# Optimization experiments

Measured on AMD Instinct MI355X. Metric: run time of the kernel, lower is better.

## Reference

```python
import jax, jax.numpy as jnp
from jax import lax
import numpy as np

# constants from module construction: segmentation_loss3D(alpha=1.0, percentile=95)
ALPHA_T = 1.0          # tversky alpha
BETA_T = 2.0 - ALPHA_T # tversky beta
EPS = 1e-5
HD_ALPHA = 2.0         # HausdorffDTLoss default alpha
BIG = 1e9              # stand-in for +inf in the min-plus distance transform


def _dt1d(f, axis):
    """Exact 1D squared Euclidean distance transform along `axis`:
    d[i] = min_j f[j] + (i - j)^2, computed as a min-plus scan over j."""
    n = f.shape[axis]
    fT = jnp.moveaxis(f, axis, 0)                      # (n, ...)
    idx = jnp.arange(n, dtype=f.dtype)
    d0 = jnp.full(fT.shape[1:] + (n,), BIG, f.dtype)   # (..., n)

    def step(d, xs):
        fj, j = xs
        return jnp.minimum(d, fj[..., None] + (idx - j) ** 2), None

    d, _ = lax.scan(step, d0, (fT, idx))
    return jnp.moveaxis(d, -1, axis)


def _edt(mask):
    """Euclidean distance to the nearest False voxel (matches scipy edt),
    over all axes except the two leading (stack, batch) axes."""
    f = jnp.where(mask, jnp.float32(BIG), jnp.float32(0.0))
    for ax in range(2, mask.ndim):
        f = _dt1d(f, ax)
    return jnp.sqrt(f)


def _distance_fields(pred, target_oh):
    # scipy loop runs edt over the full (C, X, Y, Z) array per batch element
    imgs = jnp.stack([pred, target_oh])           # (2, B, C, X, Y, Z)
    fg = imgs > 0.5
    masks = jnp.concatenate([fg, ~fg], axis=0)    # (4, B, C, X, Y, Z)
    dist = _edt(masks)
    field = dist[:2] + dist[2:]                   # fg_dist + bg_dist
    has_fg = jnp.any(fg, axis=(2, 3, 4, 5))       # (2, B) -- torch.no_grad guard
    field = jnp.where(has_fg[:, :, None, None, None, None], field, 0.0)
    field = lax.stop_gradient(field)
    return field[0], field[1]


def setup_inputs() -> dict:
    key = jax.random.key(0)
    k1, k2 = jax.random.split(key)
    B, C, X, Y, Z = 2, 8, 64, 64, 64
    inputs = jax.random.normal(k1, (B, C, X, Y, Z), dtype=jnp.float32)
    targets = jax.random.randint(k2, (B, X, Y, Z), 0, C, dtype=jnp.int32)
    return {"inputs": inputs, "targets": targets}


def reference(inputs, targets):
    C = inputs.shape[1]
    t_oh = jax.nn.one_hot(targets, C, axis=1, dtype=inputs.dtype)  # (B,C,X,Y,Z)

    # --- tversky (dice) loss ---
    probs = jax.nn.softmax(inputs, axis=1)
    red = tuple(range(2, inputs.ndim))
    tps = jnp.sum(probs * t_oh, red)
    fps = jnp.sum(probs * (1.0 - t_oh), red) * ALPHA_T
    fns = jnp.sum((1.0 - probs) * t_oh, red) * BETA_T
    score = 2.0 * tps / (2.0 * tps + fps + fns + EPS)   # (B, C)
    dice = 1.0 - jnp.mean(score, axis=0)[1:].mean()

    # --- cross entropy (mean over all voxels) ---
    logp = jax.nn.log_softmax(inputs, axis=1)
    ce = -jnp.mean(jnp.take_along_axis(logp, targets[:, None].astype(jnp.int32), axis=1))

    # --- Hausdorff distance-transform loss ---
    pred_dt, target_dt = _distance_fields(inputs, t_oh)
    pred_error = (inputs - t_oh) ** 2
    distance = pred_dt ** HD_ALPHA + target_dt ** HD_ALPHA
    hd = jnp.mean(pred_error * distance)

    return dice + ce + hd
```

## Files before the change

### kernel.cpp

```cpp
#include <hip/hip_runtime.h>

#define NVOX (64 * 64 * 64)
#define FMU (16 * NVOX)
#define FM (16 * NVOX)


__device__ __forceinline__ float unpack_val(unsigned short p) {
    int v = p & 0x7fff;
    return (v == 32767) ? 1e9f : (float)v;
}


__global__ __launch_bounds__(256) void k_zy2(const float* __restrict__ in,
                                             const int* __restrict__ tg,
                                             unsigned short* __restrict__ f) {
    __shared__ float tile[64 * 65];
    unsigned short* tile16 = (unsigned short*)tile;
    int blk = blockIdx.x;
    int src = blk >> 10;
    int s = blk & 1023;
    int b = s >> 9, c = (s >> 6) & 7, x = s & 63;
    int w = threadIdx.x >> 6;
    int lane = threadIdx.x & 63;

    const float* pin = in + (b * 8 + c) * NVOX + x * 4096;
    const int* ptg = tg + b * NVOX + x * 4096;

#pragma unroll
    for (int k = 0; k < 16; ++k) {
        int y = k * 4 + w;
        bool member;
        if (src == 0) member = pin[y * 64 + lane] > 0.5f;
        else          member = ptg[y * 64 + lane] == c;
        unsigned long long mkA = __ballot(!member);
        unsigned long long sm = member ? mkA : ~mkA;
        unsigned long long sf = sm << (63 - lane), sb = sm >> lane;
        int df = sf ? __builtin_clzll(sf) : 64;
        int db = sb ? __builtin_ctzll(sb) : 64;
        int dz = df < db ? df : db;
        float pv = (dz > 63) ? 1e9f : (float)(dz * dz);
        tile[y * 65 + lane] = member ? -pv : pv;
    }
    __syncthreads();

    float rA[16];
    bool mreg[16];
#pragma unroll
    for (int k = 0; k < 16; ++k) {
        int z = k * 4 + w;
        float sv = tile[lane * 65 + z];
        bool m = sv < 0.f;
        float pv = fabsf(sv);
        float msign = m ? -1.f : 1.f;
        unsigned long long mw = __ballot(m);
        unsigned long long xm = m ? ~mw : mw;
        unsigned long long sf = xm << (63 - lane), sb = xm >> lane;
        int df = sf ? __builtin_clzll(sf) : 64;
        int db = sb ? __builtin_ctzll(sb) : 64;
        int dopp = df < db ? df : db;
        float d = fminf(pv, (dopp > 63) ? 1e9f : (float)(dopp * dopp));
        int q = 1;
        for (int dd = 1; dd <= 63 && (float)q < d; ++dd) {
            int jl = lane - dd, jr = lane + dd;
            float cl = 1e9f, cr = 1e9f;
            if (jl >= 0) {
                float t = tile[jl * 65 + z] * msign;
                cl = (t > 0.f) ? t : 1e9f;
            }
            if (jr < 64) {
                float t = tile[jr * 65 + z] * msign;
                cr = (t > 0.f) ? t : 1e9f;
            }
            d = fminf(d, fminf(cl, cr) + (float)q);
            q += 2 * dd + 1;
        }
        rA[k] = fminf(d, 1e9f);
        mreg[k] = m;
    }
    __syncthreads();

#pragma unroll
    for (int k = 0; k < 16; ++k) {
        int z = k * 4 + w;
        int vi = (int)fminf(rA[k], 32767.f);
        tile16[lane * 65 + z] = (unsigned short)((mreg[k] ? 0x8000 : 0) | vi);
    }
    __syncthreads();

    unsigned short* out = f + (size_t)src * FMU + (b * 8 + c) * NVOX + x * 4096;
#pragma unroll
    for (int k = 0; k < 16; ++k) {
        int y = k * 4 + w;
        out[y * 64 + lane] = tile16[y * 65 + lane];
    }
}

__global__ __launch_bounds__(256) void k_xdt(unsigned short* __restrict__ f) {
    __shared__ float tile[64 * 65];
    unsigned short* tile16 = (unsigned short*)tile;
    int blk = blockIdx.x;
    int src = blk >> 10;
    int s = blk & 1023;
    int b = s >> 9, c = (s >> 6) & 7, y = s & 63;
    int w = threadIdx.x >> 6;
    int lane = threadIdx.x & 63;

    unsigned short* base = f + (size_t)src * FMU + (b * 8 + c) * NVOX + y * 64;

#pragma unroll
    for (int k = 0; k < 16; ++k) {
        int x = k * 4 + w;
        unsigned short p = base[x * 4096 + lane];
        float v = unpack_val(p);
        tile[x * 65 + lane] = (p & 0x8000) ? -v : v;
    }
    __syncthreads();

    float rA[16];
    bool mreg[16];
#pragma unroll
    for (int k = 0; k < 16; ++k) {
        int z = k * 4 + w;
        float sv = tile[lane * 65 + z];
        bool m = sv < 0.f;
        float pv = fabsf(sv);
        float msign = m ? -1.f : 1.f;
        unsigned long long mw = __ballot(m);
        unsigned long long xm = m ? ~mw : mw;
        unsigned long long sf = xm << (63 - lane), sb = xm >> lane;
        int df = sf ? __builtin_clzll(sf) : 64;
        int db = sb ? __builtin_ctzll(sb) : 64;
        int dopp = df < db ? df : db;
        float d = fminf(pv, (dopp > 63) ? 1e9f : (float)(dopp * dopp));
        int q = 1;
        for (int dd = 1; dd <= 63 && (float)q < d; ++dd) {
            int jl = lane - dd, jr = lane + dd;
            float cl = 1e9f, cr = 1e9f;
            if (jl >= 0) {
                float t = tile[jl * 65 + z] * msign;
                cl = (t > 0.f) ? t : 1e9f;
            }
            if (jr < 64) {
                float t = tile[jr * 65 + z] * msign;
                cr = (t > 0.f) ? t : 1e9f;
            }
            d = fminf(d, fminf(cl, cr) + (float)q);
            q += 2 * dd + 1;
        }
        rA[k] = fminf(d, 1e9f);
        mreg[k] = m;
    }
    __syncthreads();

#pragma unroll
    for (int k = 0; k < 16; ++k) {
        int z = k * 4 + w;
        int vi = (int)fminf(rA[k], 32767.f);
        tile16[lane * 65 + z] = (unsigned short)((mreg[k] ? 0x8000 : 0) | vi);
    }
    __syncthreads();

#pragma unroll
    for (int k = 0; k < 16; ++k) {
        int x = k * 4 + w;
        base[x * 4096 + lane] = tile16[x * 65 + lane];
    }
}

__global__ __launch_bounds__(256) void k_chds(const float* __restrict__ in,
                                              const int* __restrict__ tg,
                                              const unsigned short* __restrict__ f,
                                              float* __restrict__ statP,
                                              double* __restrict__ predS,
                                              double* __restrict__ tgtS) {
    __shared__ float part[4][27];
    __shared__ int af;
    if (threadIdx.x == 0) af = 0;
    __syncthreads();

    int blk = blockIdx.x;
    int v = blk * 256 + threadIdx.x;
    int b = v >> 18;
    int r = v & (NVOX - 1);
    int t = tg[v];
    int lane = threadIdx.x & 63;
    int wid = threadIdx.x >> 6;

    float xs[8], ex[8];
#pragma unroll
    for (int c = 0; c < 8; ++c) xs[c] = in[(b * 8 + c) * NVOX + r];
    float mx = xs[0];
#pragma unroll
    for (int c = 1; c < 8; ++c) mx = fmaxf(mx, xs[c]);
    float se = 0.f;
#pragma unroll
    for (int c = 0; c < 8; ++c) { ex[c] = expf(xs[c] - mx); se += ex[c]; }
    float inv = 1.f / se;
    float lse = mx + logf(se);
    float xt = xs[0];
#pragma unroll
    for (int c = 1; c < 8; ++c) xt = (t == c) ? xs[c] : xt;

    bool anyP = false;
    float red[17];
    float cnt[8];
#pragma unroll
    for (int c = 0; c < 8; ++c) {
        float p = ex[c] * inv;
        red[c] = p;
        red[8 + c] = (t == c) ? p : 0.f;
        cnt[c] = (float)__popcll(__ballot(t == c));
        anyP = anyP || (xs[c] > 0.5f);
    }
    red[16] = lse - xt;

#pragma unroll
    for (int k = 0; k < 17; ++k) {
        float s = red[k];
        s += __shfl_down(s, 32);
        s += __shfl_down(s, 16);
        s += __shfl_down(s, 8);
        s += __shfl_down(s, 4);
        s += __shfl_down(s, 2);
        s += __shfl_down(s, 1);
        red[k] = s;
    }
    bool wav = __any(anyP);
    if (lane == 0) {
#pragma unroll
        for (int k = 0; k < 8; ++k) part[wid][k] = red[k];
#pragma unroll
        for (int k = 0; k < 8; ++k) part[wid][8 + k] = red[8 + k];
#pragma unroll
        for (int k = 0; k < 8; ++k) part[wid][16 + k] = cnt[k];
        part[wid][24] = red[16];
        if (wav) atomicOr(&af, 1);
    }

    float e2[8];
#pragma unroll
    for (int c = 0; c < 8; ++c) {
        float e = xs[c] - ((t == c) ? 1.f : 0.f);
        e2[c] = e * e;
    }
    float accP = 0.f, accT = 0.f;
#pragma unroll
    for (int src = 0; src < 2; ++src) {
        float fmA[8], fmB[8];
#pragma unroll
        for (int c = 0; c < 8; ++c) {
            unsigned short p = f[(size_t)src * FMU + (b * 8 + c) * NVOX + r];
            float fv = unpack_val(p);
            bool member = (p & 0x8000) != 0;
            fmA[c] = member ? fv : 0.f;
            fmB[c] = member ? 0.f : fv;
        }
        float am = 0.f;
#pragma unroll
        for (int i = 0; i < 8; ++i) {
            float da = 1e9f, db = 1e9f;
#pragma unroll
            for (int j = 0; j < 8; ++j) {
                float q = (float)((i - j) * (i - j));
                da = fminf(da, fmA[j] + q);
                db = fminf(db, fmB[j] + q);
            }
            am += e2[i] * (da + db);
        }
        if (src) accT += am; else accP += am;
    }
#pragma unroll
    for (int off = 32; off >= 1; off >>= 1) {
        accP += __shfl_down(accP, off);
        accT += __shfl_down(accT, off);
    }
    if (lane == 0) { part[wid][25] = accP; part[wid][26] = accT; }
    __syncthreads();

    int j = blk & 1023;
    if (threadIdx.x < 25)
        statP[(b * 26 + threadIdx.x) * 1024 + j] =
            part[0][threadIdx.x] + part[1][threadIdx.x] +
            part[2][threadIdx.x] + part[3][threadIdx.x];
    if (threadIdx.x == 25)
        statP[(b * 26 + 25) * 1024 + j] = af ? 1.f : 0.f;
    if (threadIdx.x == 26)
        predS[blk] = (double)part[0][25] + (double)part[1][25] +
                     (double)part[2][25] + (double)part[3][25];
    if (threadIdx.x == 27)
        tgtS[blk] = (double)part[0][26] + (double)part[1][26] +
                    (double)part[2][26] + (double)part[3][26];
}

__global__ __launch_bounds__(256) void k_final3(const float* __restrict__ statP,
                                                const double* __restrict__ predS,
                                                const double* __restrict__ tgtS,
                                                float* __restrict__ out) {
    __shared__ float rs[52];
    __shared__ double rd[4];
    int tid = threadIdx.x;
    int w = tid >> 6;
    int lane = tid & 63;

    for (int row = w; row < 52; row += 4) {
        const float* p = statP + row * 1024;
        float s = 0.f;
#pragma unroll
        for (int k = 0; k < 16; ++k) s += p[k * 64 + lane];
        s += __shfl_down(s, 32);
        s += __shfl_down(s, 16);
        s += __shfl_down(s, 8);
        s += __shfl_down(s, 4);
        s += __shfl_down(s, 2);
        s += __shfl_down(s, 1);
        if (lane == 0) rs[row] = s;
    }
    {
        const double* p = (w < 2) ? (predS + w * 1024) : (tgtS + (w - 2) * 1024);
        double s = 0.0;
#pragma unroll
        for (int k = 0; k < 16; ++k) s += p[k * 64 + lane];
        s += __shfl_down(s, 32);
        s += __shfl_down(s, 16);
        s += __shfl_down(s, 8);
        s += __shfl_down(s, 4);
        s += __shfl_down(s, 2);
        s += __shfl_down(s, 1);
        if (lane == 0) rd[w] = s;
    }
    __syncthreads();

    if (tid == 0) {
        bool fP0 = rs[0 * 26 + 25] > 0.f;
        bool fP1 = rs[1 * 26 + 25] > 0.f;
        double h = (fP0 ? rd[0] : 0.0) + (fP1 ? rd[1] : 0.0) + rd[2] + rd[3];
        float dsum = 0.f;
        for (int c = 1; c < 8; ++c) {
            float sc = 0.f;
            for (int b = 0; b < 2; ++b) {
                float S1 = rs[b * 26 + c];
                float S2 = rs[b * 26 + 8 + c];
                float Nc = rs[b * 26 + 16 + c];
                sc += 2.f * S2 / (2.f * S2 + (S1 - S2) + (Nc - S2) + 1e-5f);
            }
            dsum += sc * 0.5f;
        }
        float dice = 1.f - dsum / 7.f;
        float ce = (rs[0 * 26 + 24] + rs[1 * 26 + 24]) / 524288.f;
        out[0] = dice + ce + (float)(h / 4194304.0);
    }
}

__global__ __launch_bounds__(256, 4) void k_stats(const float* __restrict__ in,
                                                  const int* __restrict__ tg,
                                                  float* __restrict__ accF,
                                                  int* __restrict__ flags) {
    int r = blockIdx.x * 256 + threadIdx.x;
    int lane = threadIdx.x & 63;
    int wid = threadIdx.x >> 6;
    __shared__ float part[4][25];
    __shared__ int af;

    for (int b = 0; b < 2; ++b) {
        int t = tg[b * NVOX + r];
        float xs[8];
#pragma unroll
        for (int c = 0; c < 8; ++c) xs[c] = in[(b * 8 + c) * NVOX + r];
        float mx = xs[0];
#pragma unroll
        for (int c = 1; c < 8; ++c) mx = fmaxf(mx, xs[c]);
        float ex[8];
        float se = 0.f;
#pragma unroll
        for (int c = 0; c < 8; ++c) { ex[c] = expf(xs[c] - mx); se += ex[c]; }
        float inv = 1.f / se;
        float lse = mx + logf(se);
        float xt = xs[0];
#pragma unroll
        for (int c = 1; c < 8; ++c) xt = (t == c) ? xs[c] : xt;
        bool anyP = false;
        float red[25];
#pragma unroll
        for (int c = 0; c < 8; ++c) {
            float p = ex[c] * inv;
            red[c] = p;
            red[8 + c] = (t == c) ? p : 0.f;
            red[16 + c] = (t == c) ? 1.f : 0.f;
            anyP = anyP || (xs[c] > 0.5f);
        }
        red[24] = lse - xt;
#pragma unroll
        for (int k = 0; k < 25; ++k) {
            float s = red[k];
            s += __shfl_down(s, 32);
            s += __shfl_down(s, 16);
            s += __shfl_down(s, 8);
            s += __shfl_down(s, 4);
            s += __shfl_down(s, 2);
            s += __shfl_down(s, 1);
            red[k] = s;
        }
        if (threadIdx.x == 0) af = 0;
        __syncthreads();
        bool wav = __any(anyP);
        if (lane == 0) {
#pragma unroll
            for (int k = 0; k < 25; ++k) part[wid][k] = red[k];
            if (wav) atomicOr(&af, 1);
        }
        __syncthreads();
        if (threadIdx.x < 25) {
            float s = part[0][threadIdx.x] + part[1][threadIdx.x] +
                      part[2][threadIdx.x] + part[3][threadIdx.x];
            atomicAdd(&accF[b * 25 + threadIdx.x], s);
        }
        if (threadIdx.x == 0 && af) atomicOr(&flags[b], 1);
        __syncthreads();
    }
}

template <int M0>
__global__ __launch_bounds__(64) void k_mask_zy(const float* __restrict__ in,
                                                const int* __restrict__ tg,
                                                float* __restrict__ f) {
    __shared__ float tile[64 * 65];
    int blk = blockIdx.x;
    int m = M0 + (blk >> 10);
    int s = blk & 1023;
    int b = s >> 9, c = (s >> 6) & 7, x = s & 63;
    int tid = threadIdx.x;

    if ((m & 1) == 0) {
        const float* src = in + (b * 8 + c) * NVOX + x * 4096;
#pragma unroll 8
        for (int k = 0; k < 64; ++k) {
            bool fg = src[k * 64 + tid] > 0.5f;
            bool hot = (m < 2) ? fg : !fg;
            tile[k * 65 + tid] = hot ? 1e9f : 0.f;
        }
    } else {
        const int* src = tg + b * NVOX + x * 4096;
#pragma unroll 8
        for (int k = 0; k < 64; ++k) {
            bool fg = (src[k * 64 + tid] == c);
            bool hot = (m < 2) ? fg : !fg;
            tile[k * 65 + tid] = hot ? 1e9f : 0.f;
        }
    }
    __syncthreads();
    {
        float* row = &tile[tid * 65];
        float g = 1000.f;
#pragma unroll 8
        for (int z = 0; z < 64; ++z) {
            float v = row[z];
            g = (v == 0.f) ? 0.f : g + 1.f;
            row[z] = g;
        }
        g = 1000.f;
#pragma unroll 8
        for (int z = 63; z >= 0; --z) {
            float gf = row[z];
            g = (gf == 0.f) ? 0.f : g + 1.f;
            float d = fminf(gf, g);
            row[z] = (d > 63.f) ? 1e9f : d * d;
        }
    }
    __syncthreads();
    float* out = f + (size_t)(blk >> 10) * FM + (b * 8 + c) * NVOX + x * 4096;
    for (int i = 0; i < 64; ++i) {
        float d0 = tile[i * 65 + tid];
        float d = d0;
        int Ri = (int)sqrtf(d0) + 1;
        Ri = (Ri > 63) ? 63 : Ri;
        for (int dd = 1; dd <= Ri; ++dd) {
            float q = (float)(dd * dd);
            int jl = i - dd, jr = i + dd;
            float cl = (jl >= 0) ? tile[jl * 65 + tid] : 1e9f;
            float cr = (jr < 64) ? tile[jr * 65 + tid] : 1e9f;
            d = fminf(d, fminf(cl, cr) + q);
        }
        out[i * 64 + tid] = fminf(d, 1e9f);
    }
}

template <int M0>
__global__ __launch_bounds__(128, 4) void k_dtx(float* __restrict__ f) {
    __shared__ float wl[128 * 65];
    int blk = blockIdx.x;
    int mi = blk >> 9;
    int s = blk & 511;
    int plane = s >> 5;
    int y0 = (s & 31) * 2;
    int tid = threadIdx.x;
    float* fb = f + (size_t)mi * FM + plane * NVOX + y0 * 64;

#pragma unroll 8
    for (int j = 0; j < 64; ++j) wl[tid * 65 + j] = fb[j * 4096 + tid];

    float* row = &wl[tid * 65];
    for (int i = 0; i < 64; ++i) {
        float d0 = row[i];
        float d = d0;
        int Ri = (int)sqrtf(d0) + 1;
        Ri = (Ri > 63) ? 63 : Ri;
        for (int dd = 1; dd <= Ri; ++dd) {
            float q = (float)(dd * dd);
            int jl = i - dd, jr = i + dd;
            float cl = (jl >= 0) ? row[jl] : 1e9f;
            float cr = (jr < 64) ? row[jr] : 1e9f;
            d = fminf(d, fminf(cl, cr) + q);
        }
        fb[i * 4096 + tid] = fminf(d, 1e9f);
    }
}

template <int M0, int NM>
__global__ __launch_bounds__(256, 4) void k_cdt_hd(const float* __restrict__ in,
                                                   const int* __restrict__ tg,
                                                   const float* __restrict__ f,
                                                   const int* __restrict__ flags,
                                                   double* __restrict__ hd) {
    int v = blockIdx.x * 256 + threadIdx.x;
    int b = v >> 18;
    int r = v & (NVOX - 1);
    int t = tg[v];

    float e2[8];
#pragma unroll
    for (int c = 0; c < 8; ++c) {
        float e = in[(b * 8 + c) * NVOX + r] - ((t == c) ? 1.f : 0.f);
        e2[c] = e * e;
    }
    float acc = 0.f;
#pragma unroll
    for (int mi = 0; mi < NM; ++mi) {
        int m = M0 + mi;
        float fl = (m & 1) ? 1.f : (flags[b] ? 1.f : 0.f);
        float fm[8];
#pragma unroll
        for (int c = 0; c < 8; ++c)
            fm[c] = f[(size_t)mi * FM + (b * 8 + c) * NVOX + r];
        float am = 0.f;
#pragma unroll
        for (int i = 0; i < 8; ++i) {
            float d = 1e9f;
#pragma unroll
            for (int j = 0; j < 8; ++j)
                d = fminf(d, fm[j] + (float)((i - j) * (i - j)));
            am += e2[i] * d;
        }
        acc += fl * am;
    }
    float ssum = acc;
    ssum += __shfl_down(ssum, 32);
    ssum += __shfl_down(ssum, 16);
    ssum += __shfl_down(ssum, 8);
    ssum += __shfl_down(ssum, 4);
    ssum += __shfl_down(ssum, 2);
    ssum += __shfl_down(ssum, 1);
    __shared__ float part[4];
    int lane = threadIdx.x & 63;
    int wid = threadIdx.x >> 6;
    if (lane == 0) part[wid] = ssum;
    __syncthreads();
    if (threadIdx.x == 0)
        atomicAdd(hd, (double)(part[0] + part[1] + part[2] + part[3]));
}

__global__ void k_final(const float* __restrict__ accF,
                        const double* __restrict__ hd,
                        float* __restrict__ out) {
    float dsum = 0.f;
    for (int c = 1; c < 8; ++c) {
        float sc = 0.f;
        for (int b = 0; b < 2; ++b) {
            float S1 = accF[b * 25 + c];
            float S2 = accF[b * 25 + 8 + c];
            float Nc = accF[b * 25 + 16 + c];
            sc += 2.f * S2 / (2.f * S2 + (S1 - S2) + (Nc - S2) + 1e-5f);
        }
        dsum += sc * 0.5f;
    }
    float dice = 1.f - dsum / 7.f;
    float ce = (accF[24] + accF[25 + 24]) / 524288.f;
    float hdv = (float)(hd[0] / 4194304.0);
    out[0] = dice + ce + hdv;
}

template <int M0, int NM>
static void run_chunk(const float* in, const int* tg, float* f,
                      const int* flags, double* hd, hipStream_t stream) {
    k_mask_zy<M0><<<NM * 1024, 64, 0, stream>>>(in, tg, f);
    k_dtx<M0><<<NM * 512, 128, 0, stream>>>(f);
    k_cdt_hd<M0, NM><<<2048, 256, 0, stream>>>(in, tg, f, flags, hd);
}

extern "C" void kernel_launch(void* const* d_in, const int* in_sizes, int n_in,
                              void* d_out, int out_size, void* d_ws, size_t ws_size,
                              hipStream_t stream) {
    const float* in = (const float*)d_in[0];
    const int* tg = (const int*)d_in[1];
    float* out = (float*)d_out;

    size_t offF = (size_t)2 * FMU * 2;
    size_t need_fast = offF + 16384 + 16384 + 52 * 1024 * 4;

    if (ws_size >= need_fast) {
        unsigned short* fu = (unsigned short*)d_ws;
        double* predS = (double*)((char*)d_ws + offF);
        double* tgtS = (double*)((char*)d_ws + offF + 16384);
        float* statP = (float*)((char*)d_ws + offF + 32768);
        k_zy2<<<2048, 256, 0, stream>>>(in, tg, fu);
        k_xdt<<<2048, 256, 0, stream>>>(fu);
        k_chds<<<2048, 256, 0, stream>>>(in, tg, fu, statP, predS, tgtS);
        k_final3<<<1, 256, 0, stream>>>(statP, predS, tgtS, out);
    } else {
        float* f = (float*)d_ws;
        size_t acc_off = ((ws_size - 256) / 256) * 256;
        char* accB = (char*)d_ws + acc_off;
        double* hd = (double*)accB;
        float* accF = (float*)(accB + 8);
        int* flags = (int*)(accB + 208);
        hipMemsetAsync(accB, 0, 256, stream);
        k_stats<<<1024, 256, 0, stream>>>(in, tg, accF, flags);
        int nm_cap = (int)(acc_off / ((size_t)FM * 4));
        if (nm_cap >= 2) {
            run_chunk<0, 2>(in, tg, f, flags, hd, stream);
            run_chunk<2, 2>(in, tg, f, flags, hd, stream);
        } else if (nm_cap >= 1) {
            run_chunk<0, 1>(in, tg, f, flags, hd, stream);
            run_chunk<1, 1>(in, tg, f, flags, hd, stream);
            run_chunk<2, 1>(in, tg, f, flags, hd, stream);
            run_chunk<3, 1>(in, tg, f, flags, hd, stream);
        }
        k_final<<<1, 1, 0, stream>>>(accF, hd, out);
    }
}
```

Before: 141.3 us.

## Vectorize packed-field IO, drop ballot pre-pass, process two voxels per thread

The 1D distance scans in k_zy2 and k_xdt drop the ballot/clz opposite-membership pre-pass. Opposite-label neighbours now count as distance zero inside the scan loop, so the same minimum is found by iterating. Loads and stores of the 16-bit packed field now move 32-bit pairs, with the shared tile padded to 66 shorts per row to match. k_chds handles two adjacent voxels per thread using float2/int2 loads, which halves the grid and the partial-sum arrays that k_final3 reduces. The trade-off is that the scan loop may now run longer for voxels whose nearest opposite voxel is far away, and each thread in k_chds holds more registers.

Result: faster. 125.7 us (-11.1%).

```diff
diff --git a/kernel.cpp b/kernel.cpp
--- a/kernel.cpp
+++ b/kernel.cpp
@@ -52,24 +52,18 @@
         bool m = sv < 0.f;
         float pv = fabsf(sv);
         float msign = m ? -1.f : 1.f;
-        unsigned long long mw = __ballot(m);
-        unsigned long long xm = m ? ~mw : mw;
-        unsigned long long sf = xm << (63 - lane), sb = xm >> lane;
-        int df = sf ? __builtin_clzll(sf) : 64;
-        int db = sb ? __builtin_ctzll(sb) : 64;
-        int dopp = df < db ? df : db;
-        float d = fminf(pv, (dopp > 63) ? 1e9f : (float)(dopp * dopp));
+        float d = pv;
         int q = 1;
         for (int dd = 1; dd <= 63 && (float)q < d; ++dd) {
             int jl = lane - dd, jr = lane + dd;
             float cl = 1e9f, cr = 1e9f;
             if (jl >= 0) {
                 float t = tile[jl * 65 + z] * msign;
-                cl = (t > 0.f) ? t : 1e9f;
+                cl = (t > 0.f) ? t : 0.f;
             }
             if (jr < 64) {
                 float t = tile[jr * 65 + z] * msign;
-                cr = (t > 0.f) ? t : 1e9f;
+                cr = (t > 0.f) ? t : 0.f;
             }
             d = fminf(d, fminf(cl, cr) + (float)q);
             q += 2 * dd + 1;
@@ -83,15 +77,18 @@
     for (int k = 0; k < 16; ++k) {
         int z = k * 4 + w;
         int vi = (int)fminf(rA[k], 32767.f);
-        tile16[lane * 65 + z] = (unsigned short)((mreg[k] ? 0x8000 : 0) | vi);
-    }
-    __syncthreads();
-
-    unsigned short* out = f + (size_t)src * FMU + (b * 8 + c) * NVOX + x * 4096;
-#pragma unroll
-    for (int k = 0; k < 16; ++k) {
-        int y = k * 4 + w;
-        out[y * 64 + lane] = tile16[y * 65 + lane];
+        tile16[lane * 66 + z] = (unsigned short)((mreg[k] ? 0x8000 : 0) | vi);
+    }
+    __syncthreads();
+
+    unsigned int* out32 =
+        (unsigned int*)(f + (size_t)src * FMU + (b * 8 + c) * NVOX + x * 4096);
+    const unsigned int* t32 = (const unsigned int*)tile16;
+    int col = lane & 31;
+#pragma unroll
+    for (int k = 0; k < 8; ++k) {
+        int y = k * 8 + w * 2 + (lane >> 5);
+        out32[y * 32 + col] = t32[y * 33 + col];
     }
 }
 
@@ -106,13 +103,19 @@
     int lane = threadIdx.x & 63;
 
     unsigned short* base = f + (size_t)src * FMU + (b * 8 + c) * NVOX + y * 64;
-
-#pragma unroll
-    for (int k = 0; k < 16; ++k) {
-        int x = k * 4 + w;
-        unsigned short p = base[x * 4096 + lane];
-        float v = unpack_val(p);
-        tile[x * 65 + lane] = (p & 0x8000) ? -v : v;
+    unsigned int* base32 = (unsigned int*)base;
+    int col = lane & 31;
+
+#pragma unroll
+    for (int k = 0; k < 8; ++k) {
+        int x = k * 8 + w * 2 + (lane >> 5);
+        unsigned int pk = base32[x * 2048 + col];
+        unsigned short p0 = (unsigned short)(pk & 0xffff);
+        unsigned short p1 = (unsigned short)(pk >> 16);
+        float v0 = unpack_val(p0), v1 = unpack_val(p1);
+        int zz = col * 2;
+        tile[x * 65 + zz] = (p0 & 0x8000) ? -v0 : v0;
+        tile[x * 65 + zz + 1] = (p1 & 0x8000) ? -v1 : v1;
     }
     __syncthreads();
 
@@ -125,24 +128,18 @@
         bool m = sv < 0.f;
         float pv = fabsf(sv);
         float msign = m ? -1.f : 1.f;
-        unsigned long long mw = __ballot(m);
-        unsigned long long xm = m ? ~mw : mw;
-        unsigned long long sf = xm << (63 - lane), sb = xm >> lane;
-        int df = sf ? __builtin_clzll(sf) : 64;
-        int db = sb ? __builtin_ctzll(sb) : 64;
-        int dopp = df < db ? df : db;
-        float d = fminf(pv, (dopp > 63) ? 1e9f : (float)(dopp * dopp));
+        float d = pv;
         int q = 1;
         for (int dd = 1; dd <= 63 && (float)q < d; ++dd) {
             int jl = lane - dd, jr = lane + dd;
             float cl = 1e9f, cr = 1e9f;
             if (jl >= 0) {
                 float t = tile[jl * 65 + z] * msign;
-                cl = (t > 0.f) ? t : 1e9f;
+                cl = (t > 0.f) ? t : 0.f;
             }
             if (jr < 64) {
                 float t = tile[jr * 65 + z] * msign;
-                cr = (t > 0.f) ? t : 1e9f;
+                cr = (t > 0.f) ? t : 0.f;
             }
             d = fminf(d, fminf(cl, cr) + (float)q);
             q += 2 * dd + 1;
@@ -156,14 +153,15 @@
     for (int k = 0; k < 16; ++k) {
         int z = k * 4 + w;
         int vi = (int)fminf(rA[k], 32767.f);
-        tile16[lane * 65 + z] = (unsigned short)((mreg[k] ? 0x8000 : 0) | vi);
-    }
-    __syncthreads();
-
-#pragma unroll
-    for (int k = 0; k < 16; ++k) {
-        int x = k * 4 + w;
-        base[x * 4096 + lane] = tile16[x * 65 + lane];
+        tile16[lane * 66 + z] = (unsigned short)((mreg[k] ? 0x8000 : 0) | vi);
+    }
+    __syncthreads();
+
+    const unsigned int* t32 = (const unsigned int*)tile16;
+#pragma unroll
+    for (int k = 0; k < 8; ++k) {
+        int x = k * 8 + w * 2 + (lane >> 5);
+        base32[x * 2048 + col] = t32[x * 33 + col];
     }
 }
 
@@ -179,40 +177,56 @@
     __syncthreads();
 
     int blk = blockIdx.x;
-    int v = blk * 256 + threadIdx.x;
+    int v = blk * 512 + threadIdx.x * 2;
     int b = v >> 18;
     int r = v & (NVOX - 1);
-    int t = tg[v];
     int lane = threadIdx.x & 63;
     int wid = threadIdx.x >> 6;
 
-    float xs[8], ex[8];
-#pragma unroll
-    for (int c = 0; c < 8; ++c) xs[c] = in[(b * 8 + c) * NVOX + r];
-    float mx = xs[0];
-#pragma unroll
-    for (int c = 1; c < 8; ++c) mx = fmaxf(mx, xs[c]);
-    float se = 0.f;
-#pragma unroll
-    for (int c = 0; c < 8; ++c) { ex[c] = expf(xs[c] - mx); se += ex[c]; }
-    float inv = 1.f / se;
-    float lse = mx + logf(se);
-    float xt = xs[0];
-#pragma unroll
-    for (int c = 1; c < 8; ++c) xt = (t == c) ? xs[c] : xt;
-
+    int2 tt = *(const int2*)&tg[v];
+    float2 xv[8];
+#pragma unroll
+    for (int c = 0; c < 8; ++c)
+        xv[c] = *(const float2*)&in[(b * 8 + c) * NVOX + r];
+
+    float red[17];
+#pragma unroll
+    for (int k = 0; k < 17; ++k) red[k] = 0.f;
     bool anyP = false;
-    float red[17];
+
+#pragma unroll
+    for (int u = 0; u < 2; ++u) {
+        int t = u ? tt.y : tt.x;
+        float xs[8];
+#pragma unroll
+        for (int c = 0; c < 8; ++c) xs[c] = u ? xv[c].y : xv[c].x;
+        float mx = xs[0];
+#pragma unroll
+        for (int c = 1; c < 8; ++c) mx = fmaxf(mx, xs[c]);
+        float ex[8];
+        float se = 0.f;
+#pragma unroll
+        for (int c = 0; c < 8; ++c) { ex[c] = expf(xs[c] - mx); se += ex[c]; }
+        float inv = 1.f / se;
+        float lse = mx + logf(se);
+        float xt = xs[0];
+#pragma unroll
+        for (int c = 1; c < 8; ++c) xt = (t == c) ? xs[c] : xt;
+#pragma unroll
+        for (int c = 0; c < 8; ++c) {
+            float p = ex[c] * inv;
+            red[c] += p;
+            red[8 + c] += (t == c) ? p : 0.f;
+            anyP = anyP || (xs[c] > 0.5f);
+        }
+        red[16] += lse - xt;
+    }
+
     float cnt[8];
 #pragma unroll
-    for (int c = 0; c < 8; ++c) {
-        float p = ex[c] * inv;
-        red[c] = p;
-        red[8 + c] = (t == c) ? p : 0.f;
-        cnt[c] = (float)__popcll(__ballot(t == c));
-        anyP = anyP || (xs[c] > 0.5f);
-    }
-    red[16] = lse - xt;
+    for (int c = 0; c < 8; ++c)
+        cnt[c] = (float)(__popcll(__ballot(tt.x == c)) +
+                         __popcll(__ballot(tt.y == c)));
 
 #pragma unroll
     for (int k = 0; k < 17; ++k) {
@@ -237,37 +251,51 @@
         if (wav) atomicOr(&af, 1);
     }
 
-    float e2[8];
-#pragma unroll
-    for (int c = 0; c < 8; ++c) {
-        float e = xs[c] - ((t == c) ? 1.f : 0.f);
-        e2[c] = e * e;
-    }
+    unsigned int fw[16];
+#pragma unroll
+    for (int src = 0; src < 2; ++src)
+#pragma unroll
+        for (int c = 0; c < 8; ++c)
+            fw[src * 8 + c] =
+                *(const unsigned int*)&f[(size_t)src * FMU + (b * 8 + c) * NVOX + r];
+
     float accP = 0.f, accT = 0.f;
 #pragma unroll
-    for (int src = 0; src < 2; ++src) {
-        float fmA[8], fmB[8];
+    for (int u = 0; u < 2; ++u) {
+        int t = u ? tt.y : tt.x;
+        float e2[8];
 #pragma unroll
         for (int c = 0; c < 8; ++c) {
-            unsigned short p = f[(size_t)src * FMU + (b * 8 + c) * NVOX + r];
-            float fv = unpack_val(p);
-            bool member = (p & 0x8000) != 0;
-            fmA[c] = member ? fv : 0.f;
-            fmB[c] = member ? 0.f : fv;
-        }
-        float am = 0.f;
-#pragma unroll
-        for (int i = 0; i < 8; ++i) {
-            float da = 1e9f, db = 1e9f;
-#pragma unroll
-            for (int j = 0; j < 8; ++j) {
-                float q = (float)((i - j) * (i - j));
-                da = fminf(da, fmA[j] + q);
-                db = fminf(db, fmB[j] + q);
+            float x = u ? xv[c].y : xv[c].x;
+            float e = x - ((t == c) ? 1.f : 0.f);
+            e2[c] = e * e;
+        }
+#pragma unroll
+        for (int src = 0; src < 2; ++src) {
+            float fmA[8], fmB[8];
+#pragma unroll
+            for (int c = 0; c < 8; ++c) {
+                unsigned int pk = fw[src * 8 + c];
+                unsigned short p = (unsigned short)(u ? (pk >> 16) : (pk & 0xffff));
+                float fv = unpack_val(p);
+                bool member = (p & 0x8000) != 0;
+                fmA[c] = member ? fv : 0.f;
+                fmB[c] = member ? 0.f : fv;
             }
-            am += e2[i] * (da + db);
-        }
-        if (src) accT += am; else accP += am;
+            float am = 0.f;
+#pragma unroll
+            for (int i = 0; i < 8; ++i) {
+                float da = 1e9f, db = 1e9f;
+#pragma unroll
+                for (int j = 0; j < 8; ++j) {
+                    float q = (float)((i - j) * (i - j));
+                    da = fminf(da, fmA[j] + q);
+                    db = fminf(db, fmB[j] + q);
+                }
+                am += e2[i] * (da + db);
+            }
+            if (src) accT += am; else accP += am;
+        }
     }
 #pragma unroll
     for (int off = 32; off >= 1; off >>= 1) {
@@ -277,13 +305,13 @@
     if (lane == 0) { part[wid][25] = accP; part[wid][26] = accT; }
     __syncthreads();
 
-    int j = blk & 1023;
+    int j = blk & 511;
     if (threadIdx.x < 25)
-        statP[(b * 26 + threadIdx.x) * 1024 + j] =
+        statP[(b * 26 + threadIdx.x) * 512 + j] =
             part[0][threadIdx.x] + part[1][threadIdx.x] +
             part[2][threadIdx.x] + part[3][threadIdx.x];
     if (threadIdx.x == 25)
-        statP[(b * 26 + 25) * 1024 + j] = af ? 1.f : 0.f;
+        statP[(b * 26 + 25) * 512 + j] = af ? 1.f : 0.f;
     if (threadIdx.x == 26)
         predS[blk] = (double)part[0][25] + (double)part[1][25] +
                      (double)part[2][25] + (double)part[3][25];
@@ -303,10 +331,10 @@
     int lane = tid & 63;
 
     for (int row = w; row < 52; row += 4) {
-        const float* p = statP + row * 1024;
+        const float* p = statP + row * 512;
         float s = 0.f;
 #pragma unroll
-        for (int k = 0; k < 16; ++k) s += p[k * 64 + lane];
+        for (int k = 0; k < 8; ++k) s += p[k * 64 + lane];
         s += __shfl_down(s, 32);
         s += __shfl_down(s, 16);
         s += __shfl_down(s, 8);
@@ -316,10 +344,10 @@
         if (lane == 0) rs[row] = s;
     }
     {
-        const double* p = (w < 2) ? (predS + w * 1024) : (tgtS + (w - 2) * 1024);
+        const double* p = (w < 2) ? (predS + w * 512) : (tgtS + (w - 2) * 512);
         double s = 0.0;
 #pragma unroll
-        for (int k = 0; k < 16; ++k) s += p[k * 64 + lane];
+        for (int k = 0; k < 8; ++k) s += p[k * 64 + lane];
         s += __shfl_down(s, 32);
         s += __shfl_down(s, 16);
         s += __shfl_down(s, 8);
@@ -604,16 +632,16 @@
     float* out = (float*)d_out;
 
     size_t offF = (size_t)2 * FMU * 2;
-    size_t need_fast = offF + 16384 + 16384 + 52 * 1024 * 4;
+    size_t need_fast = offF + 8192 + 8192 + 52 * 512 * 4;
 
     if (ws_size >= need_fast) {
         unsigned short* fu = (unsigned short*)d_ws;
         double* predS = (double*)((char*)d_ws + offF);
-        double* tgtS = (double*)((char*)d_ws + offF + 16384);
-        float* statP = (float*)((char*)d_ws + offF + 32768);
+        double* tgtS = (double*)((char*)d_ws + offF + 8192);
+        float* statP = (float*)((char*)d_ws + offF + 16384);
         k_zy2<<<2048, 256, 0, stream>>>(in, tg, fu);
         k_xdt<<<2048, 256, 0, stream>>>(fu);
-        k_chds<<<2048, 256, 0, stream>>>(in, tg, fu, statP, predS, tgtS);
+        k_chds<<<1024, 256, 0, stream>>>(in, tg, fu, statP, predS, tgtS);
         k_final3<<<1, 256, 0, stream>>>(statP, predS, tgtS, out);
     } else {
         float* f = (float*)d_ws;
```
